# Performance work log

Measured on AMD Instinct MI355X. Metric: run time of the kernel, lower is better.

## Reference

```python
import jax, jax.numpy as jnp
import numpy as np

HIDDEN = 128
NUM_GRAPHS = 16384
N_NODES = 500000
SHIFT = float(np.log(2.0))


def setup_inputs() -> dict:
    key = jax.random.key(0)
    k_v, k_b, k_w1, k_w2 = jax.random.split(key, 4)
    v = jax.random.normal(k_v, (N_NODES, HIDDEN), dtype=jnp.float32)
    batch = jnp.sort(jax.random.randint(k_b, (N_NODES,), 0, NUM_GRAPHS, dtype=jnp.int64))
    # xavier_uniform for Linear weights (torch stores [out, in]; we use [in, out])
    lim1 = float(np.sqrt(6.0 / (HIDDEN + 2 * HIDDEN)))
    W1 = jax.random.uniform(k_w1, (HIDDEN, 2 * HIDDEN), minval=-lim1, maxval=lim1, dtype=jnp.float32)
    b1 = jnp.zeros((2 * HIDDEN,), dtype=jnp.float32)
    lim2 = float(np.sqrt(6.0 / (2 * HIDDEN + 1)))
    W2 = jax.random.uniform(k_w2, (2 * HIDDEN, 1), minval=-lim2, maxval=lim2, dtype=jnp.float32)
    b2 = jnp.zeros((1,), dtype=jnp.float32)
    return {"v": v, "batch": batch, "W1": W1, "b1": b1, "W2": W2, "b2": b2}


def reference(v, batch, W1, b1, W2, b2):
    # scatter-sum readout: [n_nodes, H] -> [n_graphs, H]
    u = jax.ops.segment_sum(v, batch, num_segments=NUM_GRAPHS)
    # lin1 -> shifted softplus -> lin2
    h = jax.nn.softplus(u @ W1 + b1) - SHIFT
    return h @ W2 + b2  # [n_graphs, 1]
```

## Files before the change

kernel.cpp:

```cpp
#include <hip/hip_runtime.h>
#include <math.h>

#define HIDDEN 128
#define NGRAPH 16384
#define GPB 32
#define NBLK (NGRAPH / GPB)
#define NTHR 512

typedef __attribute__((ext_vector_type(8))) short short8;
typedef __attribute__((ext_vector_type(4))) float f32x4;

__device__ __constant__ float kSHIFT = 0.69314718055994530942f;

__device__ __forceinline__ unsigned short f2bf(float f) {
    unsigned int u = __builtin_bit_cast(unsigned int, f);
    u = (u + 0x7FFFu + ((u >> 16) & 1u)) >> 16;
    return (unsigned short)u;
}

__global__ __launch_bounds__(256) void offsets_kernel(
    const int* __restrict__ batch, int* __restrict__ offs, int n_nodes)
{
    int i = blockIdx.x * blockDim.x + threadIdx.x;
    if (i >= n_nodes) return;
    int b = batch[i];
    int prev = (i == 0) ? -1 : batch[i - 1];
    for (int g = prev + 1; g <= b; ++g) offs[g] = i;
    if (i == n_nodes - 1)
        for (int g = b + 1; g <= NGRAPH; ++g) offs[g] = n_nodes;
}

__global__ __launch_bounds__(NTHR, 4) void fused_kernel(
    const float* __restrict__ v, const int* __restrict__ offs,
    const float* __restrict__ W1, const float* __restrict__ b1,
    const float* __restrict__ W2, const float* __restrict__ b2,
    float* __restrict__ out)
{
    __shared__ short u_b[GPB * HIDDEN];
    __shared__ float red_s[8][GPB];
    __shared__ int   offs_s[GPB + 1];

    const int t  = threadIdx.x;
    const int l  = t & 63;
    const int w  = t >> 6;
    const int g0 = blockIdx.x * GPB;

    if (t < GPB + 1) offs_s[t] = offs[g0 + t];

    short8 bfrag[2][4];
    {
        const int lcol = w * 32 + (l & 15);
        #pragma unroll
        for (int ct = 0; ct < 2; ++ct) {
            const int col = lcol + ct * 16;
            #pragma unroll
            for (int kt = 0; kt < 4; ++kt) {
                const int k0 = kt * 32 + (l >> 4) * 8;
                short8 f;
                #pragma unroll
                for (int j = 0; j < 8; ++j)
                    f[j] = (short)f2bf(W1[(size_t)(k0 + j) * 256 + col]);
                bfrag[ct][kt] = f;
            }
        }
    }
    __syncthreads();

    const float2* __restrict__ v2 = reinterpret_cast<const float2*>(v);
    const int w4 = w * 4;
    const int lo = offs_s[w4];
    const int hi = offs_s[w4 + 4];
    int cur = 0;
    int bnd = offs_s[w4 + 1];
    float accx = 0.f, accy = 0.f;
    const int k2 = 2 * l;

    for (int r = lo; r < hi; r += 8) {
        float2 x[8];
        #pragma unroll
        for (int q = 0; q < 8; ++q) {
            int rq = r + q;
            rq = (rq < hi) ? rq : (hi - 1);
            x[q] = v2[(size_t)rq * 64 + l];
        }
        #pragma unroll
        for (int q = 0; q < 8; ++q) {
            if (r + q < hi) {
                while (r + q >= bnd) {
                    const int row = w4 + cur;
                    const int idx = row * HIDDEN + (k2 ^ ((row & 7) * 8));
                    unsigned int pk = (unsigned int)f2bf(accx)
                                    | ((unsigned int)f2bf(accy) << 16);
                    *reinterpret_cast<unsigned int*>(&u_b[idx]) = pk;
                    accx = 0.f; accy = 0.f;
                    ++cur;
                    bnd = offs_s[w4 + cur + 1];
                }
                accx += x[q].x; accy += x[q].y;
            }
        }
    }
    while (cur < 4) {
        const int row = w4 + cur;
        const int idx = row * HIDDEN + (k2 ^ ((row & 7) * 8));
        unsigned int pk = (unsigned int)f2bf(accx)
                        | ((unsigned int)f2bf(accy) << 16);
        *reinterpret_cast<unsigned int*>(&u_b[idx]) = pk;
        accx = 0.f; accy = 0.f;
        ++cur;
    }
    __syncthreads();

    f32x4 acc[2][2];
    #pragma unroll
    for (int rt = 0; rt < 2; ++rt)
        #pragma unroll
        for (int ct = 0; ct < 2; ++ct)
            acc[rt][ct] = (f32x4){0.f, 0.f, 0.f, 0.f};

    #pragma unroll
    for (int kt = 0; kt < 4; ++kt) {
        #pragma unroll
        for (int rt = 0; rt < 2; ++rt) {
            const int row = rt * 16 + (l & 15);
            const int k0  = kt * 32 + (l >> 4) * 8;
            short8 a = *reinterpret_cast<const short8*>(
                &u_b[row * HIDDEN + (k0 ^ ((row & 7) * 8))]);
            #pragma unroll
            for (int ct = 0; ct < 2; ++ct)
                acc[rt][ct] = __builtin_amdgcn_mfma_f32_16x16x32_bf16(
                    a, bfrag[ct][kt], acc[rt][ct], 0, 0, 0);
        }
    }

    float b1c[2], w2c[2];
    #pragma unroll
    for (int ct = 0; ct < 2; ++ct) {
        const int col = w * 32 + ct * 16 + (l & 15);
        b1c[ct] = b1[col];
        w2c[ct] = W2[col];
    }
    #pragma unroll
    for (int rt = 0; rt < 2; ++rt) {
        float p[4] = {0.f, 0.f, 0.f, 0.f};
        #pragma unroll
        for (int ct = 0; ct < 2; ++ct)
            #pragma unroll
            for (int reg = 0; reg < 4; ++reg) {
                float x = acc[rt][ct][reg] + b1c[ct];
                float h = fmaxf(x, 0.f) + log1pf(expf(-fabsf(x))) - kSHIFT;
                p[reg] = fmaf(h, w2c[ct], p[reg]);
            }
        #pragma unroll
        for (int reg = 0; reg < 4; ++reg) {
            float s = p[reg];
            s += __shfl_xor(s, 1);
            s += __shfl_xor(s, 2);
            s += __shfl_xor(s, 4);
            s += __shfl_xor(s, 8);
            if ((l & 15) == 0)
                red_s[w][rt * 16 + (l >> 4) * 4 + reg] = s;
        }
    }
    __syncthreads();

    if (t < GPB) {
        float s = (red_s[0][t] + red_s[1][t]) + (red_s[2][t] + red_s[3][t])
                + (red_s[4][t] + red_s[5][t]) + (red_s[6][t] + red_s[7][t]);
        out[g0 + t] = s + b2[0];
    }
}

extern "C" void kernel_launch(void* const* d_in, const int* in_sizes, int n_in,
                              void* d_out, int out_size, void* d_ws, size_t ws_size,
                              hipStream_t stream) {
    const float* v     = (const float*)d_in[0];
    const int*   batch = (const int*)d_in[1];
    const float* W1    = (const float*)d_in[2];
    const float* b1    = (const float*)d_in[3];
    const float* W2    = (const float*)d_in[4];
    const float* b2    = (const float*)d_in[5];
    float* out = (float*)d_out;

    const int n_nodes = in_sizes[0] / HIDDEN;
    int* offs = (int*)d_ws;

    offsets_kernel<<<(n_nodes + 255) / 256, 256, 0, stream>>>(batch, offs, n_nodes);
    fused_kernel<<<NBLK, NTHR, 0, stream>>>(v, offs, W1, b1, W2, b2, out);
}
```

Baseline: 60.27 us.

## Split block's node range evenly across waves with LDS atomic accumulation

Each wave previously summed the nodes of 4 fixed graphs, so waves with large segments set the block's latency. Now the block's whole node range is cut into 8 equal chunks, one per wave. Each wave binary-searches its starting graph and adds its partial sums into an fp32 shared buffer with atomics. A separate pass then converts that buffer to swizzled bf16 for the MFMA stage, at the cost of an extra 16KB of LDS, zero-initialization, another barrier and LDS atomic traffic.

```diff
diff --git a/kernel.cpp b/kernel.cpp
--- a/kernel.cpp
+++ b/kernel.cpp
@@ -36,6 +36,7 @@
     const float* __restrict__ W2, const float* __restrict__ b2,
     float* __restrict__ out)
 {
+    __shared__ float u_s[GPB * HIDDEN];
     __shared__ short u_b[GPB * HIDDEN];
     __shared__ float red_s[8][GPB];
     __shared__ int   offs_s[GPB + 1];
@@ -45,6 +46,9 @@
     const int w  = t >> 6;
     const int g0 = blockIdx.x * GPB;
 
+    float4* u_s4z = reinterpret_cast<float4*>(u_s);
+    u_s4z[t]       = make_float4(0.f, 0.f, 0.f, 0.f);
+    u_s4z[t + 512] = make_float4(0.f, 0.f, 0.f, 0.f);
     if (t < GPB + 1) offs_s[t] = offs[g0 + t];
 
     short8 bfrag[2][4];
@@ -67,47 +71,58 @@
     __syncthreads();
 
     const float2* __restrict__ v2 = reinterpret_cast<const float2*>(v);
-    const int w4 = w * 4;
-    const int lo = offs_s[w4];
-    const int hi = offs_s[w4 + 4];
-    int cur = 0;
-    int bnd = offs_s[w4 + 1];
-    float accx = 0.f, accy = 0.f;
-    const int k2 = 2 * l;
-
-    for (int r = lo; r < hi; r += 8) {
-        float2 x[8];
-        #pragma unroll
-        for (int q = 0; q < 8; ++q) {
-            int rq = r + q;
-            rq = (rq < hi) ? rq : (hi - 1);
-            x[q] = v2[(size_t)rq * 64 + l];
-        }
-        #pragma unroll
-        for (int q = 0; q < 8; ++q) {
-            if (r + q < hi) {
-                while (r + q >= bnd) {
-                    const int row = w4 + cur;
-                    const int idx = row * HIDDEN + (k2 ^ ((row & 7) * 8));
-                    unsigned int pk = (unsigned int)f2bf(accx)
-                                    | ((unsigned int)f2bf(accy) << 16);
-                    *reinterpret_cast<unsigned int*>(&u_b[idx]) = pk;
-                    accx = 0.f; accy = 0.f;
-                    ++cur;
-                    bnd = offs_s[w4 + cur + 1];
+    const int blo = offs_s[0];
+    const int bhi = offs_s[GPB];
+    const int cs  = (bhi - blo + 7) >> 3;
+    const int c0  = blo + w * cs;
+    const int c1  = min(c0 + cs, bhi);
+
+    if (c0 < c1) {
+        int cur = 0;
+        #pragma unroll
+        for (int step = 16; step >= 1; step >>= 1)
+            if (cur + step <= 31 && offs_s[cur + step] <= c0) cur += step;
+        int bnd = offs_s[cur + 1];
+        float accx = 0.f, accy = 0.f;
+
+        for (int r = c0; r < c1; r += 8) {
+            float2 x[8];
+            #pragma unroll
+            for (int q = 0; q < 8; ++q) {
+                int rq = r + q;
+                rq = (rq < c1) ? rq : (c1 - 1);
+                x[q] = v2[(size_t)rq * 64 + l];
+            }
+            #pragma unroll
+            for (int q = 0; q < 8; ++q) {
+                if (r + q < c1) {
+                    while (r + q >= bnd) {
+                        atomicAdd(&u_s[cur * HIDDEN + 2 * l],     accx);
+                        atomicAdd(&u_s[cur * HIDDEN + 2 * l + 1], accy);
+                        accx = 0.f; accy = 0.f;
+                        ++cur;
+                        bnd = offs_s[cur + 1];
+                    }
+                    accx += x[q].x; accy += x[q].y;
                 }
-                accx += x[q].x; accy += x[q].y;
-            }
-        }
-    }
-    while (cur < 4) {
-        const int row = w4 + cur;
-        const int idx = row * HIDDEN + (k2 ^ ((row & 7) * 8));
-        unsigned int pk = (unsigned int)f2bf(accx)
-                        | ((unsigned int)f2bf(accy) << 16);
-        *reinterpret_cast<unsigned int*>(&u_b[idx]) = pk;
-        accx = 0.f; accy = 0.f;
-        ++cur;
+            }
+        }
+        atomicAdd(&u_s[cur * HIDDEN + 2 * l],     accx);
+        atomicAdd(&u_s[cur * HIDDEN + 2 * l + 1], accy);
+    }
+    __syncthreads();
+
+    {
+        const int row = t >> 4;
+        const int e0  = (t & 15) * 8;
+        const float4 lo4 = *reinterpret_cast<const float4*>(&u_s[row * HIDDEN + e0]);
+        const float4 hi4 = *reinterpret_cast<const float4*>(&u_s[row * HIDDEN + e0 + 4]);
+        short8 pk;
+        pk[0] = (short)f2bf(lo4.x); pk[1] = (short)f2bf(lo4.y);
+        pk[2] = (short)f2bf(lo4.z); pk[3] = (short)f2bf(lo4.w);
+        pk[4] = (short)f2bf(hi4.x); pk[5] = (short)f2bf(hi4.y);
+        pk[6] = (short)f2bf(hi4.z); pk[7] = (short)f2bf(hi4.w);
+        *reinterpret_cast<short8*>(&u_b[row * HIDDEN + (e0 ^ ((row & 7) * 8))]) = pk;
     }
     __syncthreads();
 
```

After: 62.41 us. +3.5%, slower.

## Use float4 loads with two rows per wave and move W1 fragment load after segment sum

Applied to the files above, without the earlier changes.

The segment-sum loop now has each wave read two node rows per instruction with float4 loads (half-wave per row, 16 rows per iteration) instead of one row with float2 loads. The two half-wave partials are combined with a cross-lane shuffle before the bf16 write to shared memory. The W1 fragment conversion is moved after the reduction, so the loads of v are issued first and the barrier between them is removed. This trades wider, more plentiful memory requests in flight for extra shuffles and more predicated per-row work.

```diff
diff --git a/kernel.cpp b/kernel.cpp
--- a/kernel.cpp
+++ b/kernel.cpp
@@ -44,8 +44,74 @@
     const int l  = t & 63;
     const int w  = t >> 6;
     const int g0 = blockIdx.x * GPB;
+    const int w4 = w * 4;
 
     if (t < GPB + 1) offs_s[t] = offs[g0 + t];
+    __syncthreads();
+
+    const float4* __restrict__ v4 = reinterpret_cast<const float4*>(v);
+    const int qd = l & 31;
+    const int ro = l >> 5;
+    const int lo = offs_s[w4];
+    const int hi = offs_s[w4 + 4];
+    int cur = 0;
+    int bnd = offs_s[w4 + 1];
+    float4 a4 = make_float4(0.f, 0.f, 0.f, 0.f);
+
+    for (int r = lo; r < hi; r += 16) {
+        float4 x[8];
+        #pragma unroll
+        for (int jj = 0; jj < 8; ++jj) {
+            int rq = r + 2 * jj + ro;
+            rq = (rq < hi) ? rq : (hi - 1);
+            x[jj] = v4[(size_t)rq * 32 + qd];
+        }
+        #pragma unroll
+        for (int q = 0; q < 16; ++q) {
+            const int row = r + q;
+            if (row < hi) {
+                while (row >= bnd) {
+                    float4 s;
+                    s.x = a4.x + __shfl_xor(a4.x, 32);
+                    s.y = a4.y + __shfl_xor(a4.y, 32);
+                    s.z = a4.z + __shfl_xor(a4.z, 32);
+                    s.w = a4.w + __shfl_xor(a4.w, 32);
+                    if (ro == 0) {
+                        const int urow = w4 + cur;
+                        const int idx  = urow * HIDDEN + ((4 * qd) ^ ((urow & 7) * 8));
+                        uint2 pk;
+                        pk.x = (unsigned int)f2bf(s.x) | ((unsigned int)f2bf(s.y) << 16);
+                        pk.y = (unsigned int)f2bf(s.z) | ((unsigned int)f2bf(s.w) << 16);
+                        *reinterpret_cast<uint2*>(&u_b[idx]) = pk;
+                    }
+                    a4 = make_float4(0.f, 0.f, 0.f, 0.f);
+                    ++cur;
+                    bnd = offs_s[w4 + cur + 1];
+                }
+                if ((q & 1) == ro) {
+                    const float4 xx = x[q >> 1];
+                    a4.x += xx.x; a4.y += xx.y; a4.z += xx.z; a4.w += xx.w;
+                }
+            }
+        }
+    }
+    while (cur < 4) {
+        float4 s;
+        s.x = a4.x + __shfl_xor(a4.x, 32);
+        s.y = a4.y + __shfl_xor(a4.y, 32);
+        s.z = a4.z + __shfl_xor(a4.z, 32);
+        s.w = a4.w + __shfl_xor(a4.w, 32);
+        if (ro == 0) {
+            const int urow = w4 + cur;
+            const int idx  = urow * HIDDEN + ((4 * qd) ^ ((urow & 7) * 8));
+            uint2 pk;
+            pk.x = (unsigned int)f2bf(s.x) | ((unsigned int)f2bf(s.y) << 16);
+            pk.y = (unsigned int)f2bf(s.z) | ((unsigned int)f2bf(s.w) << 16);
+            *reinterpret_cast<uint2*>(&u_b[idx]) = pk;
+        }
+        a4 = make_float4(0.f, 0.f, 0.f, 0.f);
+        ++cur;
+    }
 
     short8 bfrag[2][4];
     {
@@ -66,51 +132,6 @@
     }
     __syncthreads();
 
-    const float2* __restrict__ v2 = reinterpret_cast<const float2*>(v);
-    const int w4 = w * 4;
-    const int lo = offs_s[w4];
-    const int hi = offs_s[w4 + 4];
-    int cur = 0;
-    int bnd = offs_s[w4 + 1];
-    float accx = 0.f, accy = 0.f;
-    const int k2 = 2 * l;
-
-    for (int r = lo; r < hi; r += 8) {
-        float2 x[8];
-        #pragma unroll
-        for (int q = 0; q < 8; ++q) {
-            int rq = r + q;
-            rq = (rq < hi) ? rq : (hi - 1);
-            x[q] = v2[(size_t)rq * 64 + l];
-        }
-        #pragma unroll
-        for (int q = 0; q < 8; ++q) {
-            if (r + q < hi) {
-                while (r + q >= bnd) {
-                    const int row = w4 + cur;
-                    const int idx = row * HIDDEN + (k2 ^ ((row & 7) * 8));
-                    unsigned int pk = (unsigned int)f2bf(accx)
-                                    | ((unsigned int)f2bf(accy) << 16);
-                    *reinterpret_cast<unsigned int*>(&u_b[idx]) = pk;
-                    accx = 0.f; accy = 0.f;
-                    ++cur;
-                    bnd = offs_s[w4 + cur + 1];
-                }
-                accx += x[q].x; accy += x[q].y;
-            }
-        }
-    }
-    while (cur < 4) {
-        const int row = w4 + cur;
-        const int idx = row * HIDDEN + (k2 ^ ((row & 7) * 8));
-        unsigned int pk = (unsigned int)f2bf(accx)
-                        | ((unsigned int)f2bf(accy) << 16);
-        *reinterpret_cast<unsigned int*>(&u_b[idx]) = pk;
-        accx = 0.f; accy = 0.f;
-        ++cur;
-    }
-    __syncthreads();
-
     f32x4 acc[2][2];
     #pragma unroll
     for (int rt = 0; rt < 2; ++rt)
```

New measurement: 62.83 us. 4.2% more time.
